# Kernel optimization log

Measured on AMD Instinct MI355X. Metric: run time of the kernel, lower is better.

The kernel has to match this reference:

```python
import jax, jax.numpy as jnp
import numpy as np

N, D, H, DH = 8192, 512, 8, 64          # seq len, model dim, heads, head dim
NF = int(DH * math_log) if False else 266  # nb_features = int(64 * ln(64)) = 266
EPS = 1e-4                               # performer softmax-kernel eps
LN_EPS = 1e-5


def layernorm(x, g, b):
    mu = x.mean(-1, keepdims=True)
    var = ((x - mu) ** 2).mean(-1, keepdims=True)
    return (x - mu) * jax.lax.rsqrt(var + LN_EPS) * g + b


def softmax_kernel(data, proj, is_query):
    # data: [b,h,n,dh], proj: [nf,dh] -> phi(data): [b,h,n,nf]
    dnorm = DH ** -0.25
    ratio = NF ** -0.5
    dd = jnp.einsum('bhnd,jd->bhnj', data * dnorm, proj)
    diag = (data ** 2).sum(-1, keepdims=True) * 0.5 * (dnorm ** 2)
    if is_query:
        m = jnp.max(dd, axis=-1, keepdims=True)
    else:
        m = jnp.max(dd, axis=(-1, -2), keepdims=True)
    return ratio * (jnp.exp(dd - diag - m) + EPS)


def setup_inputs() -> dict:
    key = jax.random.key(0)
    ks = jax.random.split(key, 10)
    s = 0.02
    return {
        'x': jax.random.normal(ks[0], (N, D), jnp.float32),
        'proj': jax.random.normal(ks[1], (NF, DH), jnp.float32),
        'ln1_g': jnp.ones((D,), jnp.float32), 'ln1_b': jnp.zeros((D,), jnp.float32),
        'wq': jax.random.normal(ks[2], (D, D), jnp.float32) * s,
        'wk': jax.random.normal(ks[3], (D, D), jnp.float32) * s,
        'wv': jax.random.normal(ks[4], (D, D), jnp.float32) * s,
        'wo': jax.random.normal(ks[5], (D, D), jnp.float32) * s,
        'wo_b': jnp.zeros((D,), jnp.float32),
        'ln2_g': jnp.ones((D,), jnp.float32), 'ln2_b': jnp.zeros((D,), jnp.float32),
        'w1': jax.random.normal(ks[6], (D, 4 * D), jnp.float32) * s,
        'b1': jnp.zeros((4 * D,), jnp.float32),
        'w2': jax.random.normal(ks[7], (4 * D, D), jnp.float32) * s,
        'b2': jnp.zeros((D,), jnp.float32),
    }


def reference(x, proj, ln1_g, ln1_b, wq, wk, wv, wo, wo_b, ln2_g, ln2_b, w1, b1, w2, b2):
    xb = x[None]                                     # [1,N,D] (the unsqueeze(0))
    # --- PreLN FAVOR+ self-attention ---
    h = layernorm(xb, ln1_g, ln1_b)
    def split_heads(t):
        return t.reshape(1, N, H, DH).transpose(0, 2, 1, 3)   # [1,H,N,DH]
    q = split_heads(h @ wq)
    k = split_heads(h @ wk)
    v = split_heads(h @ wv)
    qp = softmax_kernel(q, proj, True)               # [1,H,N,NF]
    kp = softmax_kernel(k, proj, False)              # [1,H,N,NF]
    # non-causal linear attention
    context = jnp.einsum('bhnj,bhnd->bhjd', kp, v)   # [1,H,NF,DH]
    d_inv = 1.0 / jnp.einsum('bhnj,bhj->bhn', qp, kp.sum(axis=2))
    attn = jnp.einsum('bhnj,bhjd->bhnd', qp, context) * d_inv[..., None]
    attn = attn.transpose(0, 2, 1, 3).reshape(1, N, D)
    xb = xb + attn @ wo + wo_b
    # --- PreLN feed-forward (GELU, mult=4) ---
    h2 = layernorm(xb, ln2_g, ln2_b)
    xb = xb + jax.nn.gelu(h2 @ w1 + b1) @ w2 + b2
    return xb[0]                                     # squeeze -> [N,D]
```

## Files before the change

kernel.cpp:

```cpp
#include <hip/hip_runtime.h>
#include <math.h>


typedef __attribute__((ext_vector_type(8))) short bf16x8;
typedef __attribute__((ext_vector_type(4))) float f32x4;

#define N_SEQ 8192
#define DMODEL 512
#define DQKV 1536
#define NHEAD 8
#define DHEAD 64
#define NF 266
#define NFP 320
#define PEPS 1e-4f
#define LNEPS 1e-5f
#define RATIO 0.06131393694f

__device__ __forceinline__ unsigned short f2bf(float f) {
  unsigned u = __float_as_uint(f);
  u += 0x7FFFu + ((u >> 16) & 1u);
  return (unsigned short)(u >> 16);
}
__device__ __forceinline__ float bf2f(unsigned short b) {
  return __uint_as_float(((unsigned)b) << 16);
}
__device__ __forceinline__ unsigned enc_f32(float f) {
  unsigned i = __float_as_uint(f);
  return (i & 0x80000000u) ? ~i : (i | 0x80000000u);
}
__device__ __forceinline__ float dec_f32(unsigned u) {
  return (u & 0x80000000u) ? __uint_as_float(u & 0x7FFFFFFFu) : __uint_as_float(~u);
}

__device__ __forceinline__ void g2l16(const void* g, void* l) {
  __builtin_amdgcn_global_load_lds(
      (const __attribute__((address_space(1))) void*)g,
      (__attribute__((address_space(3))) void*)l, 16, 0, 0);
}

template <int N>
__device__ __forceinline__ void wait_vmcnt() {
  if constexpr (N == 0) asm volatile("s_waitcnt vmcnt(0)" ::: "memory");
  else if constexpr (N == 5) asm volatile("s_waitcnt vmcnt(5)" ::: "memory");
  else if constexpr (N == 6) asm volatile("s_waitcnt vmcnt(6)" ::: "memory");
}
__device__ __forceinline__ void wait_lgkm0() {
  asm volatile("s_waitcnt lgkmcnt(0)" ::: "memory");
}


__device__ __forceinline__ void ln_row(const float* __restrict__ x,
                                       const float* __restrict__ g,
                                       const float* __restrict__ b,
                                       unsigned short* __restrict__ out,
                                       long row, int lane) {
  const float4* xr = (const float4*)(x + row * DMODEL);
  float4 v0 = xr[lane * 2], v1 = xr[lane * 2 + 1];
  float s = v0.x + v0.y + v0.z + v0.w + v1.x + v1.y + v1.z + v1.w;
  #pragma unroll
  for (int m = 32; m >= 1; m >>= 1) s += __shfl_xor(s, m);
  float mu = s * (1.0f / DMODEL);
  float d[8] = {v0.x - mu, v0.y - mu, v0.z - mu, v0.w - mu,
                v1.x - mu, v1.y - mu, v1.z - mu, v1.w - mu};
  float q = 0.f;
  #pragma unroll
  for (int k = 0; k < 8; ++k) q += d[k] * d[k];
  #pragma unroll
  for (int m = 32; m >= 1; m >>= 1) q += __shfl_xor(q, m);
  float inv = rsqrtf(q * (1.0f / DMODEL) + LNEPS);
  const float4* gr = (const float4*)g;
  const float4* br = (const float4*)b;
  float4 g0 = gr[lane * 2], g1 = gr[lane * 2 + 1];
  float4 b0 = br[lane * 2], b1 = br[lane * 2 + 1];
  float gg[8] = {g0.x, g0.y, g0.z, g0.w, g1.x, g1.y, g1.z, g1.w};
  float bb[8] = {b0.x, b0.y, b0.z, b0.w, b1.x, b1.y, b1.z, b1.w};
  unsigned short o[8];
  #pragma unroll
  for (int k = 0; k < 8; ++k) o[k] = f2bf(d[k] * inv * gg[k] + bb[k]);
  ((uint4*)(out + row * DMODEL))[lane] = *(uint4*)o;
}


__global__ __launch_bounds__(256) void prep_kernel(
    const float* __restrict__ wq, const float* __restrict__ wk,
    const float* __restrict__ wv, const float* __restrict__ wo,
    const float* __restrict__ w1, const float* __restrict__ w2,
    const float* __restrict__ proj,
    unsigned short* __restrict__ wtqkv, unsigned short* __restrict__ wot,
    unsigned short* __restrict__ w1t, unsigned short* __restrict__ w2t,
    unsigned short* __restrict__ pb, unsigned* __restrict__ mk,
    const float* __restrict__ x,
    const float* __restrict__ ln1g, const float* __restrict__ ln1b,
    unsigned short* __restrict__ h_bf) {
  int bid = blockIdx.x;
  if (bid < 3072) {
    const float* src; unsigned short* dst; int R, C, base;
    if (bid < 256)       { src = wq; dst = wtqkv;          R = 512;  C = 512;  base = 0; }
    else if (bid < 512)  { src = wk; dst = wtqkv + 262144; R = 512;  C = 512;  base = 256; }
    else if (bid < 768)  { src = wv; dst = wtqkv + 524288; R = 512;  C = 512;  base = 512; }
    else if (bid < 1024) { src = wo; dst = wot;            R = 512;  C = 512;  base = 768; }
    else if (bid < 2048) { src = w1; dst = w1t;            R = 512;  C = 2048; base = 1024; }
    else                 { src = w2; dst = w2t;            R = 2048; C = 512;  base = 2048; }
    int lb = bid - base;
    int nbx = C / 32;
    int c0 = (lb % nbx) * 32, r0 = (lb / nbx) * 32;
    __shared__ float tile[32][33];
    int tx = threadIdx.x & 31, ty = threadIdx.x >> 5;
    #pragma unroll
    for (int i = ty; i < 32; i += 8)
      tile[i][tx] = src[(long)(r0 + i) * C + c0 + tx];
    __syncthreads();
    #pragma unroll
    for (int i = ty; i < 32; i += 8)
      dst[(long)(c0 + i) * R + r0 + tx] = f2bf(tile[tx][i]);
  } else if (bid < 3152) {
    int id = (bid - 3072) * 256 + threadIdx.x;
    int j = id >> 6;
    pb[id] = (j < NF) ? f2bf(proj[(long)j * 64 + (id & 63)] * 0.35355339059327373f)
                      : (unsigned short)0;
  } else if (bid == 3152) {
    if (threadIdx.x < NHEAD) mk[threadIdx.x] = 0x007FFFFFu;
  } else {
    long row = (long)(bid - 3153) * 4 + (threadIdx.x >> 6);
    ln_row(x, ln1g, ln1b, h_bf, row, threadIdx.x & 63);
  }
}


__global__ __launch_bounds__(256) void ln_kernel(const float* __restrict__ x,
                                                 const float* __restrict__ g,
                                                 const float* __restrict__ b,
                                                 unsigned short* __restrict__ out) {
  long row = (long)blockIdx.x * 4 + (threadIdx.x >> 6);
  ln_row(x, g, b, out, row, threadIdx.x & 63);
}

enum { EPI_BF16 = 0, EPI_BIAS_RES_F32 = 2, EPI_BIAS_GELU = 3, EPI_QKV = 4 };


template <int EPI>
__global__ __launch_bounds__(512, 4) void gemm8w_kernel(
    const unsigned short* __restrict__ A, int lda,
    const unsigned short* __restrict__ Bt, int ldb,
    void* __restrict__ Cv, int ldc,
    int K,
    const float* __restrict__ bias,
    const float* __restrict__ res, int ldr,
    unsigned short* __restrict__ vt) {
  constexpr int MR = 4, NR = 2;
  constexpr int S = 5;
  const int tid = threadIdx.x;
  const int wave = tid >> 6, lane = tid & 63;
  const int lr = lane & 15, lg = lane >> 4;
  const int wr = wave >> 1, wc = wave & 1;
  const int m0 = blockIdx.x * 256, n0 = blockIdx.y * 64;

  __shared__ uint4 a_s[2][2048];
  __shared__ uint4 b_s[2][512];

  const unsigned short* asrc[4];
  #pragma unroll
  for (int e = 0; e < 4; ++e) {
    int chunk = e * 512 + tid;
    int r = chunk >> 3, c = chunk & 7;
    asrc[e] = A + (long)(m0 + r) * lda + (c ^ (r & 7)) * 8;
  }
  const unsigned short* bsrc;
  {
    int r = tid >> 3, c = tid & 7;
    bsrc = Bt + (long)(n0 + r) * ldb + (c ^ (r & 7)) * 8;
  }
  const int wbase = tid & 448;

  f32x4 acc[MR][NR] = {};

  auto stage = [&](int buf, int t) {
    #pragma unroll
    for (int e = 0; e < 4; ++e)
      g2l16(asrc[e] + t * 64, &a_s[buf][e * 512 + wbase]);
    g2l16(bsrc + t * 64, &b_s[buf][wbase]);
  };
  auto compute = [&](int buf) {
    #pragma unroll
    for (int ks = 0; ks < 2; ++ks) {
      bf16x8 af[MR], bv[NR];
      #pragma unroll
      for (int i = 0; i < MR; ++i) {
        int r = wr * 64 + i * 16 + lr;
        af[i] = *(const bf16x8*)&a_s[buf][r * 8 + ((ks * 4 + lg) ^ (r & 7))];
      }
      #pragma unroll
      for (int j = 0; j < NR; ++j) {
        int r = wc * 32 + j * 16 + lr;
        bv[j] = *(const bf16x8*)&b_s[buf][r * 8 + ((ks * 4 + lg) ^ (r & 7))];
      }
      #pragma unroll
      for (int i = 0; i < MR; ++i)
        #pragma unroll
        for (int j = 0; j < NR; ++j)
          acc[i][j] = __builtin_amdgcn_mfma_f32_16x16x32_bf16(af[i], bv[j], acc[i][j], 0, 0, 0);
    }
  };

  const int NT = K >> 6;
  stage(0, 0);
  stage(1, 1);
  wait_vmcnt<S>();
  __builtin_amdgcn_s_barrier();

  int cur = 0;
  for (int t = 0; t < NT; ++t) {
    compute(cur);
    if (t + 1 < NT) {
      wait_lgkm0();
      __builtin_amdgcn_s_barrier();
      if (t + 2 < NT) {
        stage(cur, t + 2);
        wait_vmcnt<S>();
      } else {
        wait_vmcnt<0>();
      }
      __builtin_amdgcn_s_barrier();
    }
    cur ^= 1;
  }

  #pragma unroll
  for (int i = 0; i < MR; ++i) {
    #pragma unroll
    for (int j = 0; j < NR; ++j) {
      int gn = n0 + wc * 32 + j * 16 + lr;
      int gm0 = m0 + wr * 64 + i * 16 + lg * 4;
      if (EPI == EPI_QKV && gn >= 1024) {
        int d = gn - 1024;
        uint2 u;
        u.x = (unsigned)f2bf(acc[i][j][0]) | ((unsigned)f2bf(acc[i][j][1]) << 16);
        u.y = (unsigned)f2bf(acc[i][j][2]) | ((unsigned)f2bf(acc[i][j][3]) << 16);
        *(uint2*)(vt + (long)d * N_SEQ + gm0) = u;
        continue;
      }
      #pragma unroll
      for (int rg = 0; rg < 4; ++rg) {
        int gm = gm0 + rg;
        float v = acc[i][j][rg];
        if (EPI == EPI_BF16 || EPI == EPI_QKV) {
          ((unsigned short*)Cv)[(long)gm * ldc + gn] = f2bf(v);
        } else if (EPI == EPI_BIAS_RES_F32) {
          v += bias[gn] + res[(long)gm * ldr + gn];
          ((float*)Cv)[(long)gm * ldc + gn] = v;
        } else if (EPI == EPI_BIAS_GELU) {
          v += bias[gn];
          float t3 = 0.7978845608028654f * (v + 0.044715f * v * v * v);
          v = v / (1.0f + __expf(-2.0f * t3));
          ((unsigned short*)Cv)[(long)gm * ldc + gn] = f2bf(v);
        }
      }
    }
  }
}


template <int BM, int BN, int WM, int WN, int EPI>
__global__ __launch_bounds__(256) void gemm_kernel(
    const unsigned short* __restrict__ A, int lda,
    const unsigned short* __restrict__ Bt, int ldb,
    void* __restrict__ Cv, int ldc,
    int K,
    const float* __restrict__ bias,
    const float* __restrict__ res, int ldr) {
  static_assert((BM / WM) * (BN / WN) == 4, "need 4 waves");
  constexpr int MR = WM / 16, NR = WN / 16;
  constexpr int WNN = BN / WN;
  constexpr int AIT = BM * 8 / 256;
  constexpr int BIT = BN * 8 / 256;
  constexpr int S = AIT + BIT;
  static_assert(S == 6, "wait count tuned for BM=128,BN=64");
  const int tid = threadIdx.x;
  const int wave = tid >> 6, lane = tid & 63;
  const int lr = lane & 15, lg = lane >> 4;
  const int wr = wave / WNN, wc = wave % WNN;
  const int m0 = blockIdx.x * BM, n0 = blockIdx.y * BN;

  __shared__ uint4 a_s[2][BM * 8];
  __shared__ uint4 b_s[2][BN * 8];

  const unsigned short* asrc[AIT];
  #pragma unroll
  for (int e = 0; e < AIT; ++e) {
    int chunk = e * 256 + tid;
    int r = chunk >> 3, c = chunk & 7;
    asrc[e] = A + (long)(m0 + r) * lda + (c ^ (r & 7)) * 8;
  }
  const unsigned short* bsrc[BIT];
  #pragma unroll
  for (int e = 0; e < BIT; ++e) {
    int chunk = e * 256 + tid;
    int r = chunk >> 3, c = chunk & 7;
    bsrc[e] = Bt + (long)(n0 + r) * ldb + (c ^ (r & 7)) * 8;
  }
  const int wbase = tid & 192;

  f32x4 acc[MR][NR] = {};

  auto stage = [&](int buf, int t) {
    #pragma unroll
    for (int e = 0; e < AIT; ++e)
      g2l16(asrc[e] + t * 64, &a_s[buf][e * 256 + wbase]);
    #pragma unroll
    for (int e = 0; e < BIT; ++e)
      g2l16(bsrc[e] + t * 64, &b_s[buf][e * 256 + wbase]);
  };
  auto compute = [&](int buf) {
    #pragma unroll
    for (int ks = 0; ks < 2; ++ks) {
      bf16x8 af[MR], bv[NR];
      #pragma unroll
      for (int i = 0; i < MR; ++i) {
        int r = wr * WM + i * 16 + lr;
        af[i] = *(const bf16x8*)&a_s[buf][r * 8 + ((ks * 4 + lg) ^ (r & 7))];
      }
      #pragma unroll
      for (int j = 0; j < NR; ++j) {
        int r = wc * WN + j * 16 + lr;
        bv[j] = *(const bf16x8*)&b_s[buf][r * 8 + ((ks * 4 + lg) ^ (r & 7))];
      }
      #pragma unroll
      for (int i = 0; i < MR; ++i)
        #pragma unroll
        for (int j = 0; j < NR; ++j)
          acc[i][j] = __builtin_amdgcn_mfma_f32_16x16x32_bf16(af[i], bv[j], acc[i][j], 0, 0, 0);
    }
  };

  const int NT = K >> 6;
  stage(0, 0);
  stage(1, 1);
  wait_vmcnt<6>();
  __builtin_amdgcn_s_barrier();

  int cur = 0;
  for (int t = 0; t < NT; ++t) {
    compute(cur);
    if (t + 1 < NT) {
      wait_lgkm0();
      __builtin_amdgcn_s_barrier();
      if (t + 2 < NT) {
        stage(cur, t + 2);
        wait_vmcnt<6>();
      } else {
        wait_vmcnt<0>();
      }
      __builtin_amdgcn_s_barrier();
    }
    cur ^= 1;
  }

  #pragma unroll
  for (int i = 0; i < MR; ++i) {
    #pragma unroll
    for (int j = 0; j < NR; ++j) {
      int gn = n0 + wc * WN + j * 16 + lr;
      #pragma unroll
      for (int rg = 0; rg < 4; ++rg) {
        int gm = m0 + wr * WM + i * 16 + lg * 4 + rg;
        float v = acc[i][j][rg];
        if (EPI == EPI_BF16) {
          ((unsigned short*)Cv)[(long)gm * ldc + gn] = f2bf(v);
        } else if (EPI == EPI_BIAS_RES_F32) {
          v += bias[gn] + res[(long)gm * ldr + gn];
          ((float*)Cv)[(long)gm * ldc + gn] = v;
        } else if (EPI == EPI_BIAS_GELU) {
          v += bias[gn];
          float t3 = 0.7978845608028654f * (v + 0.044715f * v * v * v);
          v = v / (1.0f + __expf(-2.0f * t3));
          ((unsigned short*)Cv)[(long)gm * ldc + gn] = f2bf(v);
        }
      }
    }
  }
}


__global__ __launch_bounds__(256) void kmax_kernel(
    const unsigned short* __restrict__ Kp,
    const unsigned short* __restrict__ pb,
    unsigned* __restrict__ mk) {
  const int tid = threadIdx.x;
  const int wave = tid >> 6, lane = tid & 63;
  const int lr = lane & 15, lg = lane >> 4;
  const int h = blockIdx.z;
  const int m0 = blockIdx.x * 256;
  const int wbase = tid & 192;

  __shared__ uint4 pbs[2560];
  __shared__ uint4 abuf[2][512];
  __shared__ float sred[4];

  #pragma unroll
  for (int e = 0; e < 10; ++e) {
    int chunk = e * 256 + tid;
    int r = chunk >> 3, c = chunk & 7;
    g2l16(pb + (long)r * DHEAD + (c ^ (r & 7)) * 8, pbs + e * 256 + wbase);
  }
  auto stage_a = [&](int b, int sub) {
    #pragma unroll
    for (int e = 0; e < 2; ++e) {
      int chunk = e * 256 + tid;
      int r = chunk >> 3, c = chunk & 7;
      g2l16(Kp + (long)(m0 + sub * 64 + r) * DQKV + h * DHEAD + (c ^ (r & 7)) * 8,
            abuf[b] + e * 256 + wbase);
    }
  };

  stage_a(0, 0);
  __syncthreads();

  float m = -3.0e38f;
  for (int sub = 0; sub < 4; ++sub) {
    const int cur = sub & 1;
    if (sub + 1 < 4) stage_a(cur ^ 1, sub + 1);

    f32x4 acc[17] = {};
    #pragma unroll
    for (int ks = 0; ks < 2; ++ks) {
      int rA = wave * 16 + lr;
      bf16x8 af = *(const bf16x8*)&abuf[cur][rA * 8 + ((ks * 4 + lg) ^ (rA & 7))];
      #pragma unroll
      for (int j = 0; j < 17; ++j) {
        int rB = j * 16 + lr;
        bf16x8 bv = *(const bf16x8*)&pbs[rB * 8 + ((ks * 4 + lg) ^ (rB & 7))];
        acc[j] = __builtin_amdgcn_mfma_f32_16x16x32_bf16(af, bv, acc[j], 0, 0, 0);
      }
    }
    #pragma unroll
    for (int j = 0; j < 17; ++j) {
      bool valid = (j < 16) || (lr < 10);
      if (valid) {
        #pragma unroll
        for (int rg = 0; rg < 4; ++rg) m = fmaxf(m, acc[j][rg]);
      }
    }
    if (sub + 1 < 4) __syncthreads();
  }

  #pragma unroll
  for (int s = 1; s < 64; s <<= 1) m = fmaxf(m, __shfl_xor(m, s));
  if (lane == 0) sred[wave] = m;
  __syncthreads();
  if (tid == 0) {
    float mm = fmaxf(fmaxf(sred[0], sred[1]), fmaxf(sred[2], sred[3]));
    atomicMax(&mk[h], enc_f32(mm));
  }
}


__global__ __launch_bounds__(256, 2) void ctx_fused_kernel(
    const unsigned short* __restrict__ Kp,
    const unsigned short* __restrict__ pb,
    const unsigned short* __restrict__ vT,
    const unsigned* __restrict__ mk,
    float* __restrict__ part,
    float* __restrict__ kspart) {
  const int tid = threadIdx.x;
  const int wave = tid >> 6, lane = tid & 63;
  const int lr = lane & 15, lg = lane >> 4;
  const int kc = blockIdx.x, h = blockIdx.y;
  const int wbase = tid & 192;

  __shared__ uint4 smem[4864];
  uint4* pbs  = smem;
  uint4* kstg = smem + 2560;
  uint4* vstg = smem + 3072;
  uint4* Pt   = smem + 3584;

  #pragma unroll
  for (int e = 0; e < 10; ++e) {
    int chunk = e * 256 + tid;
    int r = chunk >> 3, c = chunk & 7;
    g2l16(pb + (long)r * DHEAD + (c ^ (r & 7)) * 8, pbs + e * 256 + wbase);
  }

  const float mh = dec_f32(mk[h]);
  f32x4 acc2[2][10] = {};
  float colacc[20];
  #pragma unroll
  for (int j = 0; j < 20; ++j) colacc[j] = 0.f;

  const int wr = wave >> 1, wc = wave & 1;

  for (int sub = 0; sub < 4; ++sub) {
    const int n0 = kc * 256 + sub * 64;
    __syncthreads();
    #pragma unroll
    for (int e = 0; e < 2; ++e) {
      int chunk = e * 256 + tid;
      int r = chunk >> 3, c = chunk & 7;
      g2l16(Kp + (long)(n0 + r) * DQKV + h * DHEAD + (c ^ (r & 7)) * 8,
            kstg + e * 256 + wbase);
      g2l16(vT + ((long)h * DHEAD + r) * N_SEQ + n0 + (c ^ (r & 7)) * 8,
            vstg + e * 256 + wbase);
    }
    __syncthreads();

    f32x4 acc[20] = {};
    float qs = 0.f;
    #pragma unroll
    for (int ks = 0; ks < 2; ++ks) {
      int rA = wave * 16 + lr;
      bf16x8 af = *(const bf16x8*)&kstg[rA * 8 + ((ks * 4 + lg) ^ (rA & 7))];
      #pragma unroll
      for (int i = 0; i < 8; ++i) {
        float f = bf2f((unsigned short)af[i]);
        qs += f * f;
      }
      #pragma unroll
      for (int j = 0; j < 20; ++j) {
        int rB = j * 16 + lr;
        bf16x8 bv = *(const bf16x8*)&pbs[rB * 8 + ((ks * 4 + lg) ^ (rB & 7))];
        acc[j] = __builtin_amdgcn_mfma_f32_16x16x32_bf16(af, bv, acc[j], 0, 0, 0);
      }
    }
    qs += __shfl_xor(qs, 16);
    qs += __shfl_xor(qs, 32);
    float dg[4];
    #pragma unroll
    for (int rg = 0; rg < 4; ++rg) dg[rg] = 0.0625f * __shfl(qs, lg * 4 + rg);

    #pragma unroll
    for (int hf = 0; hf < 2; ++hf) {
      __syncthreads();
      unsigned short* Ptu = (unsigned short*)Pt;
      const int nrow = wave * 16 + lg * 4;
      #pragma unroll
      for (int j = hf * 10; j < hf * 10 + 10; ++j) {
        int colj = j * 16 + lr;
        int rloc = colj - hf * 160;
        #pragma unroll
        for (int rg = 0; rg < 4; ++rg) {
          float v = 0.f;
          if (colj < NF) v = RATIO * (__expf(acc[j][rg] - dg[rg] - mh) + PEPS);
          colacc[j] += v;
          int nr = nrow + rg;
          int idx = ((rloc * 8 + ((nr >> 3) ^ (rloc & 7))) << 3) + (nr & 7);
          Ptu[idx] = f2bf(v);
        }
      }
      __syncthreads();

      #pragma unroll
      for (int ks = 0; ks < 2; ++ks) {
        bf16x8 af[2], bv[5];
        #pragma unroll
        for (int i = 0; i < 2; ++i) {
          int r = wr * 32 + i * 16 + lr;
          af[i] = *(const bf16x8*)&vstg[r * 8 + ((ks * 4 + lg) ^ (r & 7))];
        }
        #pragma unroll
        for (int jj = 0; jj < 5; ++jj) {
          int r = wc * 80 + jj * 16 + lr;
          bv[jj] = *(const bf16x8*)&Pt[r * 8 + ((ks * 4 + lg) ^ (r & 7))];
        }
        #pragma unroll
        for (int i = 0; i < 2; ++i)
          #pragma unroll
          for (int jj = 0; jj < 5; ++jj)
            acc2[i][hf * 5 + jj] =
                __builtin_amdgcn_mfma_f32_16x16x32_bf16(af[i], bv[jj], acc2[i][hf * 5 + jj], 0, 0, 0);
      }
    }
  }

  float* pbase = part + ((long)(h * 32 + kc)) * 64 * NFP;
  #pragma unroll
  for (int i = 0; i < 2; ++i) {
    #pragma unroll
    for (int idx = 0; idx < 10; ++idx) {
      int hf = idx / 5, jj = idx % 5;
      int gn = hf * 160 + wc * 80 + jj * 16 + lr;
      #pragma unroll
      for (int rg = 0; rg < 4; ++rg) {
        int gm = wr * 32 + i * 16 + lg * 4 + rg;
        pbase[(long)gm * NFP + gn] = acc2[i][idx][rg];
      }
    }
  }

  __syncthreads();
  float* kls = (float*)Pt;
  #pragma unroll
  for (int j = 0; j < 20; ++j) {
    float cs = colacc[j];
    cs += __shfl_xor(cs, 16);
    cs += __shfl_xor(cs, 32);
    if (lg == 0) kls[wave * NFP + j * 16 + lr] = cs;
  }
  __syncthreads();
  for (int c0 = tid; c0 < NFP; c0 += 256) {
    kspart[((long)(h * 32 + kc)) * NFP + c0] =
        kls[c0] + kls[NFP + c0] + kls[2 * NFP + c0] + kls[3 * NFP + c0];
  }
}


__global__ void ctx_reduce_kernel(const float* __restrict__ part,
                                  const float* __restrict__ kspart,
                                  unsigned short* __restrict__ ctxpad) {
  int i = blockIdx.x * 256 + threadIdx.x;
  int h = i / (96 * NFP);
  int rem = i % (96 * NFP);
  int r = rem / NFP, j = rem % NFP;
  float s = 0.f;
  if (r < 64) {
    #pragma unroll 4
    for (int kc = 0; kc < 32; ++kc)
      s += part[((long)(h * 32 + kc)) * 64 * NFP + r * NFP + j];
  } else if (r == 64) {
    #pragma unroll 4
    for (int kc = 0; kc < 32; ++kc)
      s += kspart[((long)(h * 32 + kc)) * NFP + j];
  }
  ctxpad[i] = f2bf(s);
}


__global__ __launch_bounds__(256) void attn_fused_kernel(
    const unsigned short* __restrict__ Qp,
    const unsigned short* __restrict__ pb,
    const unsigned short* __restrict__ ctxpad,
    unsigned short* __restrict__ attn) {
  const int tid = threadIdx.x;
  const int wave = tid >> 6, lane = tid & 63;
  const int lr = lane & 15, lg = lane >> 4;
  const int h = blockIdx.z;
  const int m0 = blockIdx.x * 64;
  const int wbase = tid & 192;

  __shared__ uint4 smem[4096];
  auto sbuf = [&](int b) { return smem + b * 768; };
  uint4* Pf = smem + 1536;

  const unsigned short* Aq = Qp + (long)m0 * DQKV + h * DHEAD;
  const unsigned short* Ch = ctxpad + (long)h * 96 * NFP;

  auto stage_ctx = [&](int b, int kk) {
    #pragma unroll
    for (int e = 0; e < 3; ++e) {
      int chunk = e * 256 + tid;
      int r = chunk >> 3, c = chunk & 7;
      g2l16(Ch + (long)r * NFP + kk * 64 + (c ^ (r & 7)) * 8, sbuf(b) + e * 256 + wbase);
    }
  };

  #pragma unroll
  for (int e = 0; e < 2; ++e) {
    int chunk = e * 256 + tid;
    int r = chunk >> 3, c = chunk & 7;
    g2l16(Aq + (long)r * DQKV + (c ^ (r & 7)) * 8, sbuf(0) + e * 256 + wbase);
  }
  #pragma unroll
  for (int e = 0; e < 10; ++e) {
    int chunk = e * 256 + tid;
    int r = chunk >> 3, c = chunk & 7;
    g2l16(pb + (long)r * DHEAD + (c ^ (r & 7)) * 8, Pf + e * 256 + wbase);
  }
  __syncthreads();

  f32x4 acc[20] = {};
  float qs = 0.f;
  #pragma unroll
  for (int ks = 0; ks < 2; ++ks) {
    int rA = wave * 16 + lr;
    bf16x8 af = *(const bf16x8*)&sbuf(0)[rA * 8 + ((ks * 4 + lg) ^ (rA & 7))];
    #pragma unroll
    for (int i = 0; i < 8; ++i) {
      float f = bf2f((unsigned short)af[i]);
      qs += f * f;
    }
    #pragma unroll
    for (int j = 0; j < 20; ++j) {
      int rB = j * 16 + lr;
      bf16x8 bv = *(const bf16x8*)&Pf[rB * 8 + ((ks * 4 + lg) ^ (rB & 7))];
      acc[j] = __builtin_amdgcn_mfma_f32_16x16x32_bf16(af, bv, acc[j], 0, 0, 0);
    }
  }
  qs += __shfl_xor(qs, 16);
  qs += __shfl_xor(qs, 32);
  float dg[4];
  #pragma unroll
  for (int rg = 0; rg < 4; ++rg) dg[rg] = 0.0625f * __shfl(qs, lg * 4 + rg);

  float mrow[4];
  #pragma unroll
  for (int rg = 0; rg < 4; ++rg) mrow[rg] = -3.0e38f;
  #pragma unroll
  for (int j = 0; j < 17; ++j) {
    bool valid = (j < 16) || (lr < 10);
    if (valid) {
      #pragma unroll
      for (int rg = 0; rg < 4; ++rg) mrow[rg] = fmaxf(mrow[rg], acc[j][rg]);
    }
  }
  #pragma unroll
  for (int s = 1; s < 16; s <<= 1)
    #pragma unroll
    for (int rg = 0; rg < 4; ++rg) mrow[rg] = fmaxf(mrow[rg], __shfl_xor(mrow[rg], s));

  __syncthreads();
  stage_ctx(0, 0);

  unsigned short* Pu = (unsigned short*)Pf;
  const int prow = wave * 16 + lg * 4;
  #pragma unroll
  for (int j = 0; j < 20; ++j) {
    int col = j * 16 + lr;
    int kk = col >> 6, cc = (col >> 3) & 7;
    #pragma unroll
    for (int rg = 0; rg < 4; ++rg) {
      float v = 0.f;
      if (col < NF) v = RATIO * (__expf(acc[j][rg] - dg[rg] - mrow[rg]) + PEPS);
      int rw = prow + rg;
      int idx = ((kk * 512 + rw * 8 + (cc ^ (rw & 7))) << 3) + (col & 7);
      Pu[idx] = f2bf(v);
    }
  }
  __syncthreads();

  f32x4 acc2[6] = {};
  #pragma unroll
  for (int kk = 0; kk < 5; ++kk) {
    const int cur = kk & 1;
    if (kk + 1 < 5) stage_ctx(cur ^ 1, kk + 1);
    #pragma unroll
    for (int ks = 0; ks < 2; ++ks) {
      int rA = wave * 16 + lr;
      bf16x8 af = *(const bf16x8*)&Pf[kk * 512 + rA * 8 + ((ks * 4 + lg) ^ (rA & 7))];
      #pragma unroll
      for (int j = 0; j < 6; ++j) {
        int rB = j * 16 + lr;
        bf16x8 bv = *(const bf16x8*)&sbuf(cur)[rB * 8 + ((ks * 4 + lg) ^ (rB & 7))];
        acc2[j] = __builtin_amdgcn_mfma_f32_16x16x32_bf16(af, bv, acc2[j], 0, 0, 0);
      }
    }
    if (kk + 1 < 5) __syncthreads();
  }

  #pragma unroll
  for (int rg = 0; rg < 4; ++rg) {
    float dv = __shfl(acc2[4][rg], lane & 48);
    float inv = 1.0f / dv;
    int gm = m0 + wave * 16 + lg * 4 + rg;
    #pragma unroll
    for (int j = 0; j < 4; ++j) {
      attn[(long)gm * DMODEL + h * DHEAD + j * 16 + lr] = f2bf(acc2[j][rg] * inv);
    }
  }
}


extern "C" void kernel_launch(void* const* d_in, const int* in_sizes, int n_in,
                              void* d_out, int out_size, void* d_ws, size_t ws_size,
                              hipStream_t stream) {
  const float* x    = (const float*)d_in[0];
  const float* proj = (const float*)d_in[1];
  const float* ln1g = (const float*)d_in[2];
  const float* ln1b = (const float*)d_in[3];
  const float* wq   = (const float*)d_in[4];
  const float* wk   = (const float*)d_in[5];
  const float* wv   = (const float*)d_in[6];
  const float* wo   = (const float*)d_in[7];
  const float* wob  = (const float*)d_in[8];
  const float* ln2g = (const float*)d_in[9];
  const float* ln2b = (const float*)d_in[10];
  const float* w1   = (const float*)d_in[11];
  const float* b1   = (const float*)d_in[12];
  const float* w2   = (const float*)d_in[13];
  const float* b2   = (const float*)d_in[14];

  char* ws = (char*)d_ws;
  unsigned short* wtqkv = (unsigned short*)(ws + 0);
  unsigned short* wot   = (unsigned short*)(ws + 1572864);
  unsigned short* w1t   = (unsigned short*)(ws + 2097152);
  unsigned short* w2t   = (unsigned short*)(ws + 4194304);
  unsigned short* pb    = (unsigned short*)(ws + 6291456);
  unsigned short* h_bf  = (unsigned short*)(ws + 6332416);
  unsigned short* qkv   = (unsigned short*)(ws + 14721024);
  unsigned* mk          = (unsigned*)(ws + 124297216);
  unsigned short* vT    = (unsigned short*)(ws + 124297472);
  float* part           = (float*)(ws + 132686080);
  float* kspart         = (float*)(ws + 153657600);
  unsigned short* ctxpad= (unsigned short*)(ws + 154978560);
  unsigned short* gbf   = (unsigned short*)(ws + 130468096);
  unsigned short* attn  = h_bf;
  unsigned short* h2    = qkv;
  float* xb             = (float*)d_out;

  dim3 blk(256);

  prep_kernel<<<5201, blk, 0, stream>>>(wq, wk, wv, wo, w1, w2, proj,
                                        wtqkv, wot, w1t, w2t, pb, mk,
                                        x, ln1g, ln1b, h_bf);

  gemm8w_kernel<EPI_QKV><<<dim3(32, 24), dim3(512), 0, stream>>>(
      h_bf, 512, wtqkv, 512, qkv, DQKV, 512, nullptr, nullptr, 0, vT);

  kmax_kernel<<<dim3(32, 1, 8), blk, 0, stream>>>(qkv + 512, pb, mk);

  ctx_fused_kernel<<<dim3(32, 8), blk, 0, stream>>>(qkv + 512, pb, vT, mk, part, kspart);
  ctx_reduce_kernel<<<960, blk, 0, stream>>>(part, kspart, ctxpad);

  attn_fused_kernel<<<dim3(128, 1, 8), blk, 0, stream>>>(qkv, pb, ctxpad, attn);

  gemm_kernel<128, 64, 64, 32, EPI_BIAS_RES_F32><<<dim3(64, 8), blk, 0, stream>>>(
      attn, 512, wot, 512, xb, 512, 512, wob, x, 512);

  ln_kernel<<<2048, blk, 0, stream>>>(xb, ln2g, ln2b, h2);

  gemm8w_kernel<EPI_BIAS_GELU><<<dim3(32, 32), dim3(512), 0, stream>>>(
      h2, 512, w1t, 512, gbf, 2048, 512, b1, nullptr, 0, nullptr);

  gemm_kernel<128, 64, 64, 32, EPI_BIAS_RES_F32><<<dim3(64, 8), blk, 0, stream>>>(
      gbf, 2048, w2t, 2048, d_out, 512, 2048, b2, xb, 512);
}
```

Baseline: 168.4 us.

## Store residual stream and context partials in bf16 instead of fp32

The attention-output GEMM now writes the post-attention residual stream as bf16 to a workspace buffer rather than fp32 into the output. The second layernorm and the FFN2 residual add read that bf16 buffer. The per-chunk context partial sums are also stored as bf16 before the cross-chunk reduction. This halves the bytes for these intermediates, at the cost of precision in the residual path and in the accumulated context sums.

```diff
diff --git a/kernel.cpp b/kernel.cpp
--- a/kernel.cpp
+++ b/kernel.cpp
@@ -65,6 +65,41 @@
   float q = 0.f;
   #pragma unroll
   for (int k = 0; k < 8; ++k) q += d[k] * d[k];
+  #pragma unroll
+  for (int m = 32; m >= 1; m >>= 1) q += __shfl_xor(q, m);
+  float inv = rsqrtf(q * (1.0f / DMODEL) + LNEPS);
+  const float4* gr = (const float4*)g;
+  const float4* br = (const float4*)b;
+  float4 g0 = gr[lane * 2], g1 = gr[lane * 2 + 1];
+  float4 b0 = br[lane * 2], b1 = br[lane * 2 + 1];
+  float gg[8] = {g0.x, g0.y, g0.z, g0.w, g1.x, g1.y, g1.z, g1.w};
+  float bb[8] = {b0.x, b0.y, b0.z, b0.w, b1.x, b1.y, b1.z, b1.w};
+  unsigned short o[8];
+  #pragma unroll
+  for (int k = 0; k < 8; ++k) o[k] = f2bf(d[k] * inv * gg[k] + bb[k]);
+  ((uint4*)(out + row * DMODEL))[lane] = *(uint4*)o;
+}
+
+__device__ __forceinline__ void ln_row_bf(const unsigned short* __restrict__ x,
+                                          const float* __restrict__ g,
+                                          const float* __restrict__ b,
+                                          unsigned short* __restrict__ out,
+                                          long row, int lane) {
+  uint4 u = ((const uint4*)(x + row * DMODEL))[lane];
+  const unsigned short* e = (const unsigned short*)&u;
+  float v[8];
+  #pragma unroll
+  for (int k = 0; k < 8; ++k) v[k] = bf2f(e[k]);
+  float s = 0.f;
+  #pragma unroll
+  for (int k = 0; k < 8; ++k) s += v[k];
+  #pragma unroll
+  for (int m = 32; m >= 1; m >>= 1) s += __shfl_xor(s, m);
+  float mu = s * (1.0f / DMODEL);
+  float d[8];
+  float q = 0.f;
+  #pragma unroll
+  for (int k = 0; k < 8; ++k) { d[k] = v[k] - mu; q += d[k] * d[k]; }
   #pragma unroll
   for (int m = 32; m >= 1; m >>= 1) q += __shfl_xor(q, m);
   float inv = rsqrtf(q * (1.0f / DMODEL) + LNEPS);
@@ -127,15 +162,15 @@
 }
 
 
-__global__ __launch_bounds__(256) void ln_kernel(const float* __restrict__ x,
-                                                 const float* __restrict__ g,
-                                                 const float* __restrict__ b,
-                                                 unsigned short* __restrict__ out) {
+__global__ __launch_bounds__(256) void ln_bf_kernel(const unsigned short* __restrict__ x,
+                                                    const float* __restrict__ g,
+                                                    const float* __restrict__ b,
+                                                    unsigned short* __restrict__ out) {
   long row = (long)blockIdx.x * 4 + (threadIdx.x >> 6);
-  ln_row(x, g, b, out, row, threadIdx.x & 63);
-}
-
-enum { EPI_BF16 = 0, EPI_BIAS_RES_F32 = 2, EPI_BIAS_GELU = 3, EPI_QKV = 4 };
+  ln_row_bf(x, g, b, out, row, threadIdx.x & 63);
+}
+
+enum { EPI_BF16 = 0, EPI_BIAS_GELU = 3, EPI_QKV = 4, EPI_WO = 5, EPI_FFN2 = 6 };
 
 
 template <int EPI>
@@ -145,7 +180,6 @@
     void* __restrict__ Cv, int ldc,
     int K,
     const float* __restrict__ bias,
-    const float* __restrict__ res, int ldr,
     unsigned short* __restrict__ vt) {
   constexpr int MR = 4, NR = 2;
   constexpr int S = 5;
@@ -245,9 +279,6 @@
         float v = acc[i][j][rg];
         if (EPI == EPI_BF16 || EPI == EPI_QKV) {
           ((unsigned short*)Cv)[(long)gm * ldc + gn] = f2bf(v);
-        } else if (EPI == EPI_BIAS_RES_F32) {
-          v += bias[gn] + res[(long)gm * ldr + gn];
-          ((float*)Cv)[(long)gm * ldc + gn] = v;
         } else if (EPI == EPI_BIAS_GELU) {
           v += bias[gn];
           float t3 = 0.7978845608028654f * (v + 0.044715f * v * v * v);
@@ -267,7 +298,7 @@
     void* __restrict__ Cv, int ldc,
     int K,
     const float* __restrict__ bias,
-    const float* __restrict__ res, int ldr) {
+    const void* __restrict__ res, int ldr) {
   static_assert((BM / WM) * (BN / WN) == 4, "need 4 waves");
   constexpr int MR = WM / 16, NR = WN / 16;
   constexpr int WNN = BN / WN;
@@ -364,16 +395,12 @@
       for (int rg = 0; rg < 4; ++rg) {
         int gm = m0 + wr * WM + i * 16 + lg * 4 + rg;
         float v = acc[i][j][rg];
-        if (EPI == EPI_BF16) {
+        if (EPI == EPI_WO) {
+          v += bias[gn] + ((const float*)res)[(long)gm * ldr + gn];
           ((unsigned short*)Cv)[(long)gm * ldc + gn] = f2bf(v);
-        } else if (EPI == EPI_BIAS_RES_F32) {
-          v += bias[gn] + res[(long)gm * ldr + gn];
+        } else if (EPI == EPI_FFN2) {
+          v += bias[gn] + bf2f(((const unsigned short*)res)[(long)gm * ldr + gn]);
           ((float*)Cv)[(long)gm * ldc + gn] = v;
-        } else if (EPI == EPI_BIAS_GELU) {
-          v += bias[gn];
-          float t3 = 0.7978845608028654f * (v + 0.044715f * v * v * v);
-          v = v / (1.0f + __expf(-2.0f * t3));
-          ((unsigned short*)Cv)[(long)gm * ldc + gn] = f2bf(v);
         }
       }
     }
@@ -459,7 +486,7 @@
     const unsigned short* __restrict__ pb,
     const unsigned short* __restrict__ vT,
     const unsigned* __restrict__ mk,
-    float* __restrict__ part,
+    unsigned short* __restrict__ part,
     float* __restrict__ kspart) {
   const int tid = threadIdx.x;
   const int wave = tid >> 6, lane = tid & 63;
@@ -570,7 +597,7 @@
     }
   }
 
-  float* pbase = part + ((long)(h * 32 + kc)) * 64 * NFP;
+  unsigned short* pbase = part + ((long)(h * 32 + kc)) * 64 * NFP;
   #pragma unroll
   for (int i = 0; i < 2; ++i) {
     #pragma unroll
@@ -580,7 +607,7 @@
       #pragma unroll
       for (int rg = 0; rg < 4; ++rg) {
         int gm = wr * 32 + i * 16 + lg * 4 + rg;
-        pbase[(long)gm * NFP + gn] = acc2[i][idx][rg];
+        pbase[(long)gm * NFP + gn] = f2bf(acc2[i][idx][rg]);
       }
     }
   }
@@ -602,7 +629,7 @@
 }
 
 
-__global__ void ctx_reduce_kernel(const float* __restrict__ part,
+__global__ void ctx_reduce_kernel(const unsigned short* __restrict__ part,
                                   const float* __restrict__ kspart,
                                   unsigned short* __restrict__ ctxpad) {
   int i = blockIdx.x * 256 + threadIdx.x;
@@ -613,7 +640,7 @@
   if (r < 64) {
     #pragma unroll 4
     for (int kc = 0; kc < 32; ++kc)
-      s += part[((long)(h * 32 + kc)) * 64 * NFP + r * NFP + j];
+      s += bf2f(part[((long)(h * 32 + kc)) * 64 * NFP + r * NFP + j]);
   } else if (r == 64) {
     #pragma unroll 4
     for (int kc = 0; kc < 32; ++kc)
@@ -784,15 +811,15 @@
   unsigned short* pb    = (unsigned short*)(ws + 6291456);
   unsigned short* h_bf  = (unsigned short*)(ws + 6332416);
   unsigned short* qkv   = (unsigned short*)(ws + 14721024);
+  unsigned short* xb_bf = (unsigned short*)(ws + 39886848);
   unsigned* mk          = (unsigned*)(ws + 124297216);
   unsigned short* vT    = (unsigned short*)(ws + 124297472);
-  float* part           = (float*)(ws + 132686080);
+  unsigned short* part  = (unsigned short*)(ws + 132686080);
   float* kspart         = (float*)(ws + 153657600);
   unsigned short* ctxpad= (unsigned short*)(ws + 154978560);
   unsigned short* gbf   = (unsigned short*)(ws + 130468096);
   unsigned short* attn  = h_bf;
   unsigned short* h2    = qkv;
-  float* xb             = (float*)d_out;
 
   dim3 blk(256);
 
@@ -801,7 +828,7 @@
                                         x, ln1g, ln1b, h_bf);
 
   gemm8w_kernel<EPI_QKV><<<dim3(32, 24), dim3(512), 0, stream>>>(
-      h_bf, 512, wtqkv, 512, qkv, DQKV, 512, nullptr, nullptr, 0, vT);
+      h_bf, 512, wtqkv, 512, qkv, DQKV, 512, nullptr, vT);
 
   kmax_kernel<<<dim3(32, 1, 8), blk, 0, stream>>>(qkv + 512, pb, mk);
 
@@ -810,14 +837,14 @@
 
   attn_fused_kernel<<<dim3(128, 1, 8), blk, 0, stream>>>(qkv, pb, ctxpad, attn);
 
-  gemm_kernel<128, 64, 64, 32, EPI_BIAS_RES_F32><<<dim3(64, 8), blk, 0, stream>>>(
-      attn, 512, wot, 512, xb, 512, 512, wob, x, 512);
-
-  ln_kernel<<<2048, blk, 0, stream>>>(xb, ln2g, ln2b, h2);
+  gemm_kernel<128, 64, 64, 32, EPI_WO><<<dim3(64, 8), blk, 0, stream>>>(
+      attn, 512, wot, 512, xb_bf, 512, 512, wob, x, 512);
+
+  ln_bf_kernel<<<2048, blk, 0, stream>>>(xb_bf, ln2g, ln2b, h2);
 
   gemm8w_kernel<EPI_BIAS_GELU><<<dim3(32, 32), dim3(512), 0, stream>>>(
-      h2, 512, w1t, 512, gbf, 2048, 512, b1, nullptr, 0, nullptr);
-
-  gemm_kernel<128, 64, 64, 32, EPI_BIAS_RES_F32><<<dim3(64, 8), blk, 0, stream>>>(
-      gbf, 2048, w2t, 2048, d_out, 512, 2048, b2, xb, 512);
-}
+      h2, 512, w1t, 512, gbf, 2048, 512, b1, nullptr);
+
+  gemm_kernel<128, 64, 64, 32, EPI_FFN2><<<dim3(64, 8), blk, 0, stream>>>(
+      gbf, 2048, w2t, 2048, d_out, 512, 2048, b2, xb_bf, 512);
+}
```

Measured after the change: 163.8 us. -2.7%, faster.
